# Kernel optimization log

Measured on AMD Instinct MI355X. Metric: run time of the kernel, lower is better.

The kernel has to match this reference:

```python
import jax, jax.numpy as jnp
import numpy as np

N = 50000
E = 800000
IN_DIM = 512
HID = 64
OUT = 64
HEADS = 4
NEG_SLOPE = 0.2


def setup_inputs() -> dict:
    key = jax.random.key(0)
    ks = jax.random.split(key, 16)
    s = 0.05
    inp = {
        "x": jax.random.normal(ks[0], (N, IN_DIM), jnp.float32),
        "edge_index": jax.random.randint(ks[1], (2, E), 0, N, jnp.int64),
        # layer 1: in=512 -> heads*hid = 4*64 = 256, concat=True
        "W1l": jax.random.normal(ks[2], (IN_DIM, HEADS * HID), jnp.float32) * s,
        "b1l": jnp.zeros((HEADS * HID,), jnp.float32),
        "W1r": jax.random.normal(ks[3], (IN_DIM, HEADS * HID), jnp.float32) * s,
        "b1r": jnp.zeros((HEADS * HID,), jnp.float32),
        "att1": jax.random.normal(ks[4], (HEADS, HID), jnp.float32) * s,
        "bias1": jnp.zeros((HEADS * HID,), jnp.float32),
        # layer 2: in=256 -> heads*(2*out) = 4*128, concat=False (mean heads)
        "W2l": jax.random.normal(ks[5], (HEADS * HID, HEADS * 2 * OUT), jnp.float32) * s,
        "b2l": jnp.zeros((HEADS * 2 * OUT,), jnp.float32),
        "W2r": jax.random.normal(ks[6], (HEADS * HID, HEADS * 2 * OUT), jnp.float32) * s,
        "b2r": jnp.zeros((HEADS * 2 * OUT,), jnp.float32),
        "att2": jax.random.normal(ks[7], (HEADS, 2 * OUT), jnp.float32) * s,
        "bias2": jnp.zeros((2 * OUT,), jnp.float32),
    }
    return inp


def _gatv2(x, src, dst, Wl, bl, Wr, br, att, bias, concat):
    """GATv2Conv (PyG semantics): message x_l[src], attention over incoming edges per dst."""
    H, C = att.shape
    n = x.shape[0]
    xl = (x @ Wl + bl).reshape(n, H, C)  # source transform (messages)
    xr = (x @ Wr + br).reshape(n, H, C)  # target transform
    g = jax.nn.leaky_relu(xl[src] + xr[dst], NEG_SLOPE)   # [E, H, C]
    e = jnp.einsum('ehc,hc->eh', g, att)                  # [E, H]
    # numerically-stable softmax over irregular neighbor sets (segmented by dst)
    m = jax.ops.segment_max(e, dst, num_segments=n)
    ex = jnp.exp(e - m[dst])
    denom = jax.ops.segment_sum(ex, dst, num_segments=n)
    alpha = ex / (denom[dst] + 1e-16)                     # [E, H]
    out = jax.ops.segment_sum(xl[src] * alpha[..., None], dst, num_segments=n)  # [N, H, C]
    if concat:
        return out.reshape(n, H * C) + bias
    return out.mean(axis=1) + bias


def reference(x, edge_index, W1l, b1l, W1r, b1r, att1, bias1,
              W2l, b2l, W2r, b2r, att2, bias2):
    # add self loops (PyG add_self_loops=True default)
    loops = jnp.arange(N, dtype=edge_index.dtype)
    src = jnp.concatenate([edge_index[0], loops])
    dst = jnp.concatenate([edge_index[1], loops])
    h = jax.nn.relu(_gatv2(x, src, dst, W1l, b1l, W1r, b1r, att1, bias1, concat=True))
    return _gatv2(h, src, dst, W2l, b2l, W2r, b2r, att2, bias2, concat=False)
```

## Files before the change

### kernel.cpp

```cpp
#include <hip/hip_runtime.h>

#define NNODES 50000
#define NEDGES 800000
#define ET (NEDGES + NNODES)
#define HEADS 4

typedef __attribute__((ext_vector_type(8))) short bf16x8;
typedef __attribute__((ext_vector_type(4))) float f32x4;

#define EXP2F(x) __builtin_amdgcn_exp2f(x)

__device__ inline unsigned short f2bf(float f) {
  union { float f; unsigned int i; } c; c.f = f;
  unsigned int b = c.i + 0x7fffu + ((c.i >> 16) & 1u);
  return (unsigned short)(b >> 16);
}
__device__ inline float4 b4tof(uint2 r) {
  float4 f;
  union { unsigned int i; float v; } c;
  c.i = r.x << 16;          f.x = c.v;
  c.i = r.x & 0xffff0000u;  f.y = c.v;
  c.i = r.y << 16;          f.z = c.v;
  c.i = r.y & 0xffff0000u;  f.w = c.v;
  return f;
}


__global__ void k_hist(const int* __restrict__ ei, int* __restrict__ deg) {
  int i = blockIdx.x * blockDim.x + threadIdx.x;
  if (i >= ET) return;
  int dst = (i < NEDGES) ? ei[NEDGES + i] : (i - NEDGES);
  atomicAdd(&deg[dst], 1);
}

__global__ void k_scan1(const int* __restrict__ deg, int* __restrict__ part,
                        int* __restrict__ bsum, int n) {
  __shared__ int s[256];
  int tid = threadIdx.x;
  int i = blockIdx.x * 256 + tid;
  int v = (i < n) ? deg[i] : 0;
  s[tid] = v;
  __syncthreads();
  for (int off = 1; off < 256; off <<= 1) {
    int t = (tid >= off) ? s[tid - off] : 0;
    __syncthreads();
    s[tid] += t;
    __syncthreads();
  }
  if (i < n) part[i] = s[tid] - v;
  if (tid == 255) bsum[blockIdx.x] = s[255];
}

__global__ void k_scan2(int* bsum, int nb) {
  __shared__ int s[256];
  int t = threadIdx.x;
  int v = (t < nb) ? bsum[t] : 0;
  s[t] = v;
  __syncthreads();
  for (int off = 1; off < 256; off <<= 1) {
    int tv = (t >= off) ? s[t - off] : 0;
    __syncthreads();
    s[t] += tv;
    __syncthreads();
  }
  if (t < nb) bsum[t] = s[t] - v;
}

__global__ void k_scan3(const int* __restrict__ part, const int* __restrict__ bsum,
                        int* __restrict__ rowstart, int* __restrict__ cursor,
                        int n, int total) {
  int i = blockIdx.x * blockDim.x + threadIdx.x;
  if (i < n) {
    int v = part[i] + bsum[i >> 8];
    rowstart[i] = v;
    cursor[i] = v;
  }
  if (i == n) rowstart[n] = total;
}

__global__ void k_scatter(const int* __restrict__ ei, int* __restrict__ cursor,
                          int* __restrict__ csrsrc) {
  int i = blockIdx.x * blockDim.x + threadIdx.x;
  if (i >= ET) return;
  int src, dst;
  if (i < NEDGES) { src = ei[i]; dst = ei[NEDGES + i]; }
  else            { src = dst = i - NEDGES; }
  int pos = atomicAdd(&cursor[dst], 1);
  csrsrc[pos] = src;
}


__global__ void k_cast_bf16(const float* __restrict__ in, unsigned short* __restrict__ out, int n4) {
  int i = blockIdx.x * blockDim.x + threadIdx.x;
  if (i >= n4) return;
  float4 v = ((const float4*)in)[i];
  ushort4 o;
  o.x = f2bf(v.x); o.y = f2bf(v.y); o.z = f2bf(v.z); o.w = f2bf(v.w);
  ((ushort4*)out)[i] = o;
}

__global__ void k_castw_t(const float* __restrict__ W, unsigned short* __restrict__ Wt,
                          int K, int N) {
  int id = blockIdx.x * blockDim.x + threadIdx.x;
  if (id >= K * N) return;
  int k = id / N, n = id - k * N;
  Wt[n * K + k] = f2bf(W[id]);
}


__global__ __launch_bounds__(256) void k_gemm_mfma(
    const unsigned short* __restrict__ A, const unsigned short* __restrict__ Bt,
    const float* __restrict__ bias, unsigned short* __restrict__ C,
    int M, int K, int N) {
  __shared__ unsigned short As[128][40];
  __shared__ unsigned short Bs[128][40];
  int tid = threadIdx.x;
  int lane = tid & 63, wave = tid >> 6;
  int wr = (wave >> 1) * 64, wc = (wave & 1) * 64;
  int row0 = blockIdx.x * 128, col0 = blockIdx.y * 128;
  int fr = lane & 15;
  int fq = lane >> 4;
  int sr = tid >> 2;
  int sc = (tid & 3) * 8;

  f32x4 acc[4][4] = {};

  for (int k0 = 0; k0 < K; k0 += 32) {
#pragma unroll
    for (int q = 0; q < 2; ++q) {
      int r = sr + q * 64;
      int grow = row0 + r;
      uint4 av = make_uint4(0, 0, 0, 0);
      if (grow < M) av = *(const uint4*)&A[(size_t)grow * K + k0 + sc];
      *(uint4*)&As[r][sc] = av;
      uint4 bv = *(const uint4*)&Bt[(size_t)(col0 + r) * K + k0 + sc];
      *(uint4*)&Bs[r][sc] = bv;
    }
    __syncthreads();
    bf16x8 af[4], bfr[4];
#pragma unroll
    for (int m = 0; m < 4; ++m)
      af[m] = *(const bf16x8*)&As[wr + m * 16 + fr][fq * 8];
#pragma unroll
    for (int n = 0; n < 4; ++n)
      bfr[n] = *(const bf16x8*)&Bs[wc + n * 16 + fr][fq * 8];
#pragma unroll
    for (int m = 0; m < 4; ++m)
#pragma unroll
      for (int n = 0; n < 4; ++n)
        acc[m][n] = __builtin_amdgcn_mfma_f32_16x16x32_bf16(af[m], bfr[n], acc[m][n], 0, 0, 0);
    __syncthreads();
  }

#pragma unroll
  for (int m = 0; m < 4; ++m) {
#pragma unroll
    for (int n = 0; n < 4; ++n) {
      int col = col0 + wc + n * 16 + fr;
      float bv = bias[col];
#pragma unroll
      for (int j = 0; j < 4; ++j) {
        int row = row0 + wr + m * 16 + fq * 4 + j;
        if (row < M) C[(size_t)row * N + col] = f2bf(acc[m][n][j] + bv);
      }
    }
  }
}


#define DEFER_THR 11.0f

template <int CQ, int MODE>
__global__ __launch_bounds__(256) void k_fused(
    const int* __restrict__ rowstart, const int* __restrict__ csrsrc,
    const unsigned short* __restrict__ xl, const unsigned short* __restrict__ xr,
    const float* __restrict__ att, const float* __restrict__ bias,
    void* __restrict__ outp) {
  const int C = CQ * 64;
  const size_t RS = (size_t)HEADS * C;
  int dst = (blockIdx.x * blockDim.x + threadIdx.x) >> 6;
  int lane = threadIdx.x & 63;
  if (dst >= NNODES) return;
  int h = lane >> 4;
  int l = lane & 15;
  const int choff = h * C + l * 4;

  float4 xrv[CQ], attv[CQ];
#pragma unroll
  for (int q = 0; q < CQ; ++q) {
    xrv[q] = b4tof(*(const uint2*)&xr[(size_t)dst * RS + choff + q * 64]);
    float4 a = *(const float4*)&att[choff + q * 64];
    a.x *= 1.44269504f; a.y *= 1.44269504f;
    a.z *= 1.44269504f; a.w *= 1.44269504f;
    attv[q] = a;
  }

  int rs = rowstart[dst], re = rowstart[dst + 1];
  float m = -1e30f, den = 0.f;
  float4 acc[CQ];
#pragma unroll
  for (int q = 0; q < CQ; ++q) acc[q] = make_float4(0.f, 0.f, 0.f, 0.f);

  int src = csrsrc[rs];
  uint2 rv[CQ];
  {
    const unsigned short* p0 = &xl[(size_t)src * RS + choff];
#pragma unroll
    for (int q = 0; q < CQ; ++q) rv[q] = *(const uint2*)&p0[q * 64];
  }

  for (int i = rs; i < re; ++i) {
    int nsrc = csrsrc[(i + 1 < re) ? (i + 1) : i];
    uint2 nrv[CQ];
    {
      const unsigned short* pn = &xl[(size_t)nsrc * RS + choff];
#pragma unroll
      for (int q = 0; q < CQ; ++q) nrv[q] = *(const uint2*)&pn[q * 64];
    }
    float4 xv[CQ];
#pragma unroll
    for (int q = 0; q < CQ; ++q) xv[q] = b4tof(rv[q]);

    float p = 0.f;
#pragma unroll
    for (int q = 0; q < CQ; ++q) {
      float s;
      s = xv[q].x + xrv[q].x; p = fmaf(attv[q].x, fmaxf(s, 0.2f * s), p);
      s = xv[q].y + xrv[q].y; p = fmaf(attv[q].y, fmaxf(s, 0.2f * s), p);
      s = xv[q].z + xrv[q].z; p = fmaf(attv[q].z, fmaxf(s, 0.2f * s), p);
      s = xv[q].w + xrv[q].w; p = fmaf(attv[q].w, fmaxf(s, 0.2f * s), p);
    }
    p += __shfl_xor(p, 1);
    p += __shfl_xor(p, 2);
    p += __shfl_xor(p, 4);
    p += __shfl_xor(p, 8);

    if (__all(p <= m + DEFER_THR)) {
      float w = EXP2F(p - m);
      den += w;
#pragma unroll
      for (int q = 0; q < CQ; ++q) {
        acc[q].x = fmaf(w, xv[q].x, acc[q].x);
        acc[q].y = fmaf(w, xv[q].y, acc[q].y);
        acc[q].z = fmaf(w, xv[q].z, acc[q].z);
        acc[q].w = fmaf(w, xv[q].w, acc[q].w);
      }
    } else {
      float mn = fmaxf(m, p);
      float c1 = EXP2F(m - mn);
      float w  = EXP2F(p - mn);
      den = den * c1 + w;
#pragma unroll
      for (int q = 0; q < CQ; ++q) {
        acc[q].x = fmaf(acc[q].x, c1, w * xv[q].x);
        acc[q].y = fmaf(acc[q].y, c1, w * xv[q].y);
        acc[q].z = fmaf(acc[q].z, c1, w * xv[q].z);
        acc[q].w = fmaf(acc[q].w, c1, w * xv[q].w);
      }
      m = mn;
    }
#pragma unroll
    for (int q = 0; q < CQ; ++q) rv[q] = nrv[q];
  }

  float inv = 1.f / (den + 1e-16f);

  if (MODE == 0) {
    unsigned short* out = (unsigned short*)outp;
#pragma unroll
    for (int q = 0; q < CQ; ++q) {
      const float4 bv = *(const float4*)&bias[choff + q * 64];
      ushort4 o;
      o.x = f2bf(fmaxf(acc[q].x * inv + bv.x, 0.f));
      o.y = f2bf(fmaxf(acc[q].y * inv + bv.y, 0.f));
      o.z = f2bf(fmaxf(acc[q].z * inv + bv.z, 0.f));
      o.w = f2bf(fmaxf(acc[q].w * inv + bv.w, 0.f));
      *(ushort4*)&out[(size_t)dst * RS + choff + q * 64] = o;
    }
  } else {
    float* out = (float*)outp;
    float r[CQ][4];
#pragma unroll
    for (int q = 0; q < CQ; ++q) {
      r[q][0] = acc[q].x * inv; r[q][1] = acc[q].y * inv;
      r[q][2] = acc[q].z * inv; r[q][3] = acc[q].w * inv;
    }
#pragma unroll
    for (int q = 0; q < CQ; ++q)
#pragma unroll
      for (int j = 0; j < 4; ++j) {
        r[q][j] += __shfl_xor(r[q][j], 16);
        r[q][j] += __shfl_xor(r[q][j], 32);
      }
    if (lane < 16 * CQ) {
      int q = lane >> 4;
      int c = lane * 4;
      float4 o;
      o.x = r[q][0] * 0.25f + bias[c + 0];
      o.y = r[q][1] * 0.25f + bias[c + 1];
      o.z = r[q][2] * 0.25f + bias[c + 2];
      o.w = r[q][3] * 0.25f + bias[c + 3];
      *(float4*)&out[(size_t)dst * C + c] = o;
    }
  }
}


extern "C" void kernel_launch(void* const* d_in, const int* in_sizes, int n_in,
                              void* d_out, int out_size, void* d_ws, size_t ws_size,
                              hipStream_t stream) {
  (void)in_sizes; (void)n_in; (void)out_size; (void)ws_size;
  const float* x     = (const float*)d_in[0];
  const int*   ei    = (const int*)d_in[1];
  const float* W1l   = (const float*)d_in[2];
  const float* b1l   = (const float*)d_in[3];
  const float* W1r   = (const float*)d_in[4];
  const float* b1r   = (const float*)d_in[5];
  const float* att1  = (const float*)d_in[6];
  const float* bias1 = (const float*)d_in[7];
  const float* W2l   = (const float*)d_in[8];
  const float* b2l   = (const float*)d_in[9];
  const float* W2r   = (const float*)d_in[10];
  const float* b2r   = (const float*)d_in[11];
  const float* att2  = (const float*)d_in[12];
  const float* bias2 = (const float*)d_in[13];
  float* out = (float*)d_out;

  char* ws = (char*)d_ws;
  size_t off = 0;
  auto alloc = [&](size_t bytes) {
    char* p = ws + off;
    off = (off + bytes + 255) & ~(size_t)255;
    return p;
  };
  int*  deg      = (int*)alloc((size_t)NNODES * 4);
  int*  part     = (int*)alloc((size_t)NNODES * 4);
  int*  bsum     = (int*)alloc(256 * 4);
  int*  rowstart = (int*)alloc((size_t)(NNODES + 1) * 4);
  int*  cursor   = (int*)alloc((size_t)NNODES * 4);
  int*  csrsrc   = (int*)alloc((size_t)ET * 4);
  unsigned short* xb   = (unsigned short*)alloc((size_t)NNODES * 512 * 2);
  unsigned short* w1lt = (unsigned short*)alloc((size_t)512 * 256 * 2);
  unsigned short* w1rt = (unsigned short*)alloc((size_t)512 * 256 * 2);
  unsigned short* w2lt = (unsigned short*)alloc((size_t)256 * 512 * 2);
  unsigned short* w2rt = (unsigned short*)alloc((size_t)256 * 512 * 2);
  unsigned short* xl1  = (unsigned short*)alloc((size_t)NNODES * 256 * 2);
  unsigned short* xr1  = (unsigned short*)alloc((size_t)NNODES * 256 * 2);
  unsigned short* hbuf = (unsigned short*)alloc((size_t)NNODES * 256 * 2);
  unsigned short* xl2  = (unsigned short*)alloc((size_t)NNODES * 512 * 2);
  unsigned short* xr2  = (unsigned short*)alloc((size_t)NNODES * 512 * 2);

  (void)hipMemsetAsync(deg, 0, (size_t)NNODES * 4, stream);
  k_hist<<<(ET + 255) / 256, 256, 0, stream>>>(ei, deg);
  int nb = (NNODES + 255) / 256;
  k_scan1<<<nb, 256, 0, stream>>>(deg, part, bsum, NNODES);
  k_scan2<<<1, 256, 0, stream>>>(bsum, nb);
  k_scan3<<<(NNODES + 256) / 256, 256, 0, stream>>>(part, bsum, rowstart, cursor, NNODES, ET);
  k_scatter<<<(ET + 255) / 256, 256, 0, stream>>>(ei, cursor, csrsrc);

  k_cast_bf16<<<(NNODES * 512 / 4 + 255) / 256, 256, 0, stream>>>(x, xb, NNODES * 512 / 4);
  k_castw_t<<<(512 * 256 + 255) / 256, 256, 0, stream>>>(W1l, w1lt, 512, 256);
  k_castw_t<<<(512 * 256 + 255) / 256, 256, 0, stream>>>(W1r, w1rt, 512, 256);
  k_castw_t<<<(256 * 512 + 255) / 256, 256, 0, stream>>>(W2l, w2lt, 256, 512);
  k_castw_t<<<(256 * 512 + 255) / 256, 256, 0, stream>>>(W2r, w2rt, 256, 512);

  const int gridM = (NNODES + 127) / 128;
  const int gridFused = (NNODES + 3) / 4;

  k_gemm_mfma<<<dim3(gridM, 2), 256, 0, stream>>>(xb, w1lt, b1l, xl1, NNODES, 512, 256);
  k_gemm_mfma<<<dim3(gridM, 2), 256, 0, stream>>>(xb, w1rt, b1r, xr1, NNODES, 512, 256);
  k_fused<1, 0><<<gridFused, 256, 0, stream>>>(rowstart, csrsrc, xl1, xr1, att1, bias1, hbuf);

  k_gemm_mfma<<<dim3(gridM, 4), 256, 0, stream>>>(hbuf, w2lt, b2l, xl2, NNODES, 256, 512);
  k_gemm_mfma<<<dim3(gridM, 4), 256, 0, stream>>>(hbuf, w2rt, b2r, xr2, NNODES, 256, 512);
  k_fused<2, 1><<<gridFused, 256, 0, stream>>>(rowstart, csrsrc, xl2, xr2, att2, bias2, out);
}
```

Baseline: 556.2 us.

## Merge left/right projection GEMMs and load GEMM tiles directly into LDS

Result: faster. 504.8 us (-9.2%).

```diff
diff --git a/kernel.cpp b/kernel.cpp
--- a/kernel.cpp
+++ b/kernel.cpp
@@ -9,6 +9,10 @@
 typedef __attribute__((ext_vector_type(4))) float f32x4;
 
 #define EXP2F(x) __builtin_amdgcn_exp2f(x)
+
+#define GLOAD16(g, l) __builtin_amdgcn_global_load_lds(                      \
+    (const __attribute__((address_space(1))) unsigned int*)(g),              \
+    (__attribute__((address_space(3))) unsigned int*)(l), 16, 0, 0)
 
 __device__ inline unsigned short f2bf(float f) {
   union { float f; unsigned int i; } c; c.f = f;
@@ -99,21 +103,29 @@
   ((ushort4*)out)[i] = o;
 }
 
-__global__ void k_castw_t(const float* __restrict__ W, unsigned short* __restrict__ Wt,
-                          int K, int N) {
+__global__ void k_castw_all(const float* __restrict__ W1l, const float* __restrict__ W1r,
+                            const float* __restrict__ W2l, const float* __restrict__ W2r,
+                            unsigned short* __restrict__ w1t, unsigned short* __restrict__ w2t) {
   int id = blockIdx.x * blockDim.x + threadIdx.x;
-  if (id >= K * N) return;
-  int k = id / N, n = id - k * N;
-  Wt[n * K + k] = f2bf(W[id]);
-}
-
-
-__global__ __launch_bounds__(256) void k_gemm_mfma(
+  int which = blockIdx.y;
+  const float* W;
+  unsigned short* T;
+  int K, Nw, noff;
+  if (which == 0)      { W = W1l; T = w1t; K = 512; Nw = 256; noff = 0; }
+  else if (which == 1) { W = W1r; T = w1t; K = 512; Nw = 256; noff = 256; }
+  else if (which == 2) { W = W2l; T = w2t; K = 256; Nw = 512; noff = 0; }
+  else                 { W = W2r; T = w2t; K = 256; Nw = 512; noff = 512; }
+  int k = id / Nw, n = id - k * Nw;
+  T[(size_t)(n + noff) * K + k] = f2bf(W[id]);
+}
+
+
+__global__ __launch_bounds__(256) void k_gemm(
     const unsigned short* __restrict__ A, const unsigned short* __restrict__ Bt,
-    const float* __restrict__ bias, unsigned short* __restrict__ C,
-    int M, int K, int N) {
-  __shared__ unsigned short As[128][40];
-  __shared__ unsigned short Bs[128][40];
+    const float* __restrict__ bL, const float* __restrict__ bR, int nsplit,
+    unsigned short* __restrict__ C, int M, int K, int N) {
+  __shared__ unsigned short As[128 * 32];
+  __shared__ unsigned short Bs[128 * 32];
   int tid = threadIdx.x;
   int lane = tid & 63, wave = tid >> 6;
   int wr = (wave >> 1) * 64, wc = (wave & 1) * 64;
@@ -123,27 +135,30 @@
   int sr = tid >> 2;
   int sc = (tid & 3) * 8;
 
+  const unsigned short* ga0 = &A[(size_t)(row0 + sr) * K + sc];
+  const unsigned short* ga1 = &A[(size_t)(row0 + sr + 64) * K + sc];
+  const unsigned short* gb0 = &Bt[(size_t)(col0 + sr) * K + sc];
+  const unsigned short* gb1 = &Bt[(size_t)(col0 + sr + 64) * K + sc];
+  unsigned short* la0 = &As[tid * 8];
+  unsigned short* la1 = &As[2048 + tid * 8];
+  unsigned short* lb0 = &Bs[tid * 8];
+  unsigned short* lb1 = &Bs[2048 + tid * 8];
+
   f32x4 acc[4][4] = {};
 
   for (int k0 = 0; k0 < K; k0 += 32) {
-#pragma unroll
-    for (int q = 0; q < 2; ++q) {
-      int r = sr + q * 64;
-      int grow = row0 + r;
-      uint4 av = make_uint4(0, 0, 0, 0);
-      if (grow < M) av = *(const uint4*)&A[(size_t)grow * K + k0 + sc];
-      *(uint4*)&As[r][sc] = av;
-      uint4 bv = *(const uint4*)&Bt[(size_t)(col0 + r) * K + k0 + sc];
-      *(uint4*)&Bs[r][sc] = bv;
-    }
+    GLOAD16(ga0 + k0, la0);
+    GLOAD16(ga1 + k0, la1);
+    GLOAD16(gb0 + k0, lb0);
+    GLOAD16(gb1 + k0, lb1);
     __syncthreads();
     bf16x8 af[4], bfr[4];
 #pragma unroll
     for (int m = 0; m < 4; ++m)
-      af[m] = *(const bf16x8*)&As[wr + m * 16 + fr][fq * 8];
+      af[m] = *(const bf16x8*)&As[(wr + m * 16 + fr) * 32 + fq * 8];
 #pragma unroll
     for (int n = 0; n < 4; ++n)
-      bfr[n] = *(const bf16x8*)&Bs[wc + n * 16 + fr][fq * 8];
+      bfr[n] = *(const bf16x8*)&Bs[(wc + n * 16 + fr) * 32 + fq * 8];
 #pragma unroll
     for (int m = 0; m < 4; ++m)
 #pragma unroll
@@ -157,7 +172,7 @@
 #pragma unroll
     for (int n = 0; n < 4; ++n) {
       int col = col0 + wc + n * 16 + fr;
-      float bv = bias[col];
+      float bv = (col < nsplit) ? bL[col] : bR[col - nsplit];
 #pragma unroll
       for (int j = 0; j < 4; ++j) {
         int row = row0 + wr + m * 16 + fq * 4 + j;
@@ -170,14 +185,13 @@
 
 #define DEFER_THR 11.0f
 
-template <int CQ, int MODE>
+template <int CQ, int MODE, int STR>
 __global__ __launch_bounds__(256) void k_fused(
     const int* __restrict__ rowstart, const int* __restrict__ csrsrc,
-    const unsigned short* __restrict__ xl, const unsigned short* __restrict__ xr,
+    const unsigned short* __restrict__ xlr,
     const float* __restrict__ att, const float* __restrict__ bias,
     void* __restrict__ outp) {
   const int C = CQ * 64;
-  const size_t RS = (size_t)HEADS * C;
   int dst = (blockIdx.x * blockDim.x + threadIdx.x) >> 6;
   int lane = threadIdx.x & 63;
   if (dst >= NNODES) return;
@@ -188,7 +202,7 @@
   float4 xrv[CQ], attv[CQ];
 #pragma unroll
   for (int q = 0; q < CQ; ++q) {
-    xrv[q] = b4tof(*(const uint2*)&xr[(size_t)dst * RS + choff + q * 64]);
+    xrv[q] = b4tof(*(const uint2*)&xlr[(size_t)dst * STR + STR / 2 + choff + q * 64]);
     float4 a = *(const float4*)&att[choff + q * 64];
     a.x *= 1.44269504f; a.y *= 1.44269504f;
     a.z *= 1.44269504f; a.w *= 1.44269504f;
@@ -204,7 +218,7 @@
   int src = csrsrc[rs];
   uint2 rv[CQ];
   {
-    const unsigned short* p0 = &xl[(size_t)src * RS + choff];
+    const unsigned short* p0 = &xlr[(size_t)src * STR + choff];
 #pragma unroll
     for (int q = 0; q < CQ; ++q) rv[q] = *(const uint2*)&p0[q * 64];
   }
@@ -213,7 +227,7 @@
     int nsrc = csrsrc[(i + 1 < re) ? (i + 1) : i];
     uint2 nrv[CQ];
     {
-      const unsigned short* pn = &xl[(size_t)nsrc * RS + choff];
+      const unsigned short* pn = &xlr[(size_t)nsrc * STR + choff];
 #pragma unroll
       for (int q = 0; q < CQ; ++q) nrv[q] = *(const uint2*)&pn[q * 64];
     }
@@ -275,7 +289,7 @@
       o.y = f2bf(fmaxf(acc[q].y * inv + bv.y, 0.f));
       o.z = f2bf(fmaxf(acc[q].z * inv + bv.z, 0.f));
       o.w = f2bf(fmaxf(acc[q].w * inv + bv.w, 0.f));
-      *(ushort4*)&out[(size_t)dst * RS + choff + q * 64] = o;
+      *(ushort4*)&out[(size_t)dst * (HEADS * C) + choff + q * 64] = o;
     }
   } else {
     float* out = (float*)outp;
@@ -340,15 +354,11 @@
   int*  cursor   = (int*)alloc((size_t)NNODES * 4);
   int*  csrsrc   = (int*)alloc((size_t)ET * 4);
   unsigned short* xb   = (unsigned short*)alloc((size_t)NNODES * 512 * 2);
-  unsigned short* w1lt = (unsigned short*)alloc((size_t)512 * 256 * 2);
-  unsigned short* w1rt = (unsigned short*)alloc((size_t)512 * 256 * 2);
-  unsigned short* w2lt = (unsigned short*)alloc((size_t)256 * 512 * 2);
-  unsigned short* w2rt = (unsigned short*)alloc((size_t)256 * 512 * 2);
-  unsigned short* xl1  = (unsigned short*)alloc((size_t)NNODES * 256 * 2);
-  unsigned short* xr1  = (unsigned short*)alloc((size_t)NNODES * 256 * 2);
+  unsigned short* w1t  = (unsigned short*)alloc((size_t)512 * 512 * 2);
+  unsigned short* w2t  = (unsigned short*)alloc((size_t)1024 * 256 * 2);
+  unsigned short* xlr1 = (unsigned short*)alloc((size_t)NNODES * 512 * 2);
   unsigned short* hbuf = (unsigned short*)alloc((size_t)NNODES * 256 * 2);
-  unsigned short* xl2  = (unsigned short*)alloc((size_t)NNODES * 512 * 2);
-  unsigned short* xr2  = (unsigned short*)alloc((size_t)NNODES * 512 * 2);
+  unsigned short* xlr2 = (unsigned short*)alloc((size_t)NNODES * 1024 * 2);
 
   (void)hipMemsetAsync(deg, 0, (size_t)NNODES * 4, stream);
   k_hist<<<(ET + 255) / 256, 256, 0, stream>>>(ei, deg);
@@ -359,19 +369,14 @@
   k_scatter<<<(ET + 255) / 256, 256, 0, stream>>>(ei, cursor, csrsrc);
 
   k_cast_bf16<<<(NNODES * 512 / 4 + 255) / 256, 256, 0, stream>>>(x, xb, NNODES * 512 / 4);
-  k_castw_t<<<(512 * 256 + 255) / 256, 256, 0, stream>>>(W1l, w1lt, 512, 256);
-  k_castw_t<<<(512 * 256 + 255) / 256, 256, 0, stream>>>(W1r, w1rt, 512, 256);
-  k_castw_t<<<(256 * 512 + 255) / 256, 256, 0, stream>>>(W2l, w2lt, 256, 512);
-  k_castw_t<<<(256 * 512 + 255) / 256, 256, 0, stream>>>(W2r, w2rt, 256, 512);
+  k_castw_all<<<dim3(512, 4), 256, 0, stream>>>(W1l, W1r, W2l, W2r, w1t, w2t);
 
   const int gridM = (NNODES + 127) / 128;
   const int gridFused = (NNODES + 3) / 4;
 
-  k_gemm_mfma<<<dim3(gridM, 2), 256, 0, stream>>>(xb, w1lt, b1l, xl1, NNODES, 512, 256);
-  k_gemm_mfma<<<dim3(gridM, 2), 256, 0, stream>>>(xb, w1rt, b1r, xr1, NNODES, 512, 256);
-  k_fused<1, 0><<<gridFused, 256, 0, stream>>>(rowstart, csrsrc, xl1, xr1, att1, bias1, hbuf);
-
-  k_gemm_mfma<<<dim3(gridM, 4), 256, 0, stream>>>(hbuf, w2lt, b2l, xl2, NNODES, 256, 512);
-  k_gemm_mfma<<<dim3(gridM, 4), 256, 0, stream>>>(hbuf, w2rt, b2r, xr2, NNODES, 256, 512);
-  k_fused<2, 1><<<gridFused, 256, 0, stream>>>(rowstart, csrsrc, xl2, xr2, att2, bias2, out);
-}
+  k_gemm<<<dim3(gridM, 4), 256, 0, stream>>>(xb, w1t, b1l, b1r, 256, xlr1, NNODES, 512, 512);
+  k_fused<1, 0, 512><<<gridFused, 256, 0, stream>>>(rowstart, csrsrc, xlr1, att1, bias1, hbuf);
+
+  k_gemm<<<dim3(gridM, 8), 256, 0, stream>>>(hbuf, w2t, b2l, b2r, 512, xlr2, NNODES, 256, 1024);
+  k_fused<2, 1, 1024><<<gridFused, 256, 0, stream>>>(rowstart, csrsrc, xlr2, att2, bias2, out);
+}
```
